# Kernel tuning notes

Hardware: AMD Instinct MI355X
Metric: run time of the kernel (lower is better)

Reference implementation:

```python
import jax, jax.numpy as jnp
from jax import lax
import numpy as np

DIM = 512      # latent channel dim
K = 1024       # codebook size
KS = 320       # conv kernel size (== stride -> non-overlapping frames)
STRIDE = 320
B, L = 16, 160000  # 10s of 16kHz audio


def setup_inputs() -> dict:
    key = jax.random.key(0)
    ks = jax.random.split(key, 8)
    wav = jax.random.normal(ks[0], (B, 1, L), jnp.float32)
    enc_w = jax.random.normal(ks[1], (DIM, 1, KS), jnp.float32) * 0.05
    enc_b = jnp.zeros((DIM,), jnp.float32)
    codebook = jax.random.normal(ks[2], (K, DIM), jnp.float32)
    lin_w = jax.random.normal(ks[3], (DIM, DIM), jnp.float32) * 0.02
    lin_b = jnp.zeros((DIM,), jnp.float32)
    film_w = jax.random.normal(ks[4], (2 * DIM, DIM), jnp.float32) * 0.02
    film_b = jnp.zeros((2 * DIM,), jnp.float32)
    dec_w = jax.random.normal(ks[5], (DIM, 1, KS), jnp.float32) * 0.05
    dec_b = jnp.zeros((1,), jnp.float32)
    return dict(wav=wav, enc_w=enc_w, enc_b=enc_b, codebook=codebook,
                lin_w=lin_w, lin_b=lin_b, film_w=film_w, film_b=film_b,
                dec_w=dec_w, dec_b=dec_b)


def reference(wav, enc_w, enc_b, codebook, lin_w, lin_b, film_w, film_b, dec_w, dec_b):
    # --- NAC encoder: strided Conv1d, wav [B,1,L] -> emb [B,D,T] ---
    emb = lax.conv_general_dilated(
        wav, enc_w, window_strides=(STRIDE,), padding='VALID',
        dimension_numbers=('NCH', 'OIH', 'NCH')) + enc_b[None, :, None]

    # --- time-averaged embedding for conditioning ---
    time_avg = emb.mean(axis=-1)  # [B, D]

    # --- VQ encode: nearest codebook entry per frame ---
    x = emb.transpose(0, 2, 1)  # [B, T, D]
    # squared L2 distances [B, T, K]
    dist = (x * x).sum(-1, keepdims=True) \
         - 2.0 * jnp.einsum('btd,kd->btk', x, codebook) \
         + (codebook * codebook).sum(-1)
    codes = jnp.argmin(dist, axis=-1)  # [B, T] int

    # --- VQ decode: codebook gather ---
    emb_r = codebook[codes].transpose(0, 2, 1)  # [B, D, T]

    # --- linear on pooled embedding ---
    cond = time_avg @ lin_w.T + lin_b  # [B, D]

    # --- FiLM modulation: gamma * x + beta per channel ---
    gb = cond @ film_w.T + film_b      # [B, 2D]
    gamma, beta = jnp.split(gb, 2, axis=-1)
    modulated = gamma[:, :, None] * emb_r + beta[:, :, None]  # [B, D, T]

    # --- NAC decoder: transposed Conv1d back to waveform [B,1,L] ---
    out = lax.conv_transpose(
        modulated, dec_w, strides=(STRIDE,), padding='VALID',
        dimension_numbers=('NCH', 'IOH', 'NCH')) + dec_b[None, :, None]
    return out
```

## Files before the change

kernel.cpp:

```cpp
#include <hip/hip_runtime.h>

#define FR   8000
#define FRP  8192
#define DD   512
#define CK   1024
#define KSZ  320
#define TT   500
#define NB   16

typedef unsigned int u32;
typedef unsigned short u16;
typedef __attribute__((ext_vector_type(8))) short b8;
typedef __attribute__((ext_vector_type(4))) float f4;

__device__ __forceinline__ float bf2f(u16 h) {
    u32 u = ((u32)h) << 16;
    return __builtin_bit_cast(float, u);
}
__device__ __forceinline__ u16 f2bf(float f) {
    u32 u = __builtin_bit_cast(u32, f);
    u32 r = u + 0x7FFFu + ((u >> 16) & 1u);
    return (u16)(r >> 16);
}

__device__ __forceinline__ void gld16(const u16* g, u16* s) {
    __builtin_amdgcn_global_load_lds(
        (const __attribute__((address_space(1))) u32*)g,
        (__attribute__((address_space(3))) u32*)s, 16, 0, 0);
}

__device__ __forceinline__ f4 mfma(b8 a, b8 b, f4 c) {
    return __builtin_amdgcn_mfma_f32_16x16x32_bf16(a, b, c, 0, 0, 0);
}

__device__ __forceinline__ void split8(float4 a, float4 b, u16* dh, u16* dl) {
    float xs[8] = {a.x, a.y, a.z, a.w, b.x, b.y, b.z, b.w};
    union { u16 u[8]; b8 v; } H, L;
#pragma unroll
    for (int i = 0; i < 8; ++i) {
        u16 h = f2bf(xs[i]);
        H.u[i] = h;
        L.u[i] = f2bf(xs[i] - bf2f(h));
    }
    *(b8*)dh = H.v;
    *(b8*)dl = L.v;
}

__global__ __launch_bounds__(256) void k_prep(const float* __restrict__ enc_w,
                                              u16* __restrict__ ewh, u16* __restrict__ ewl,
                                              const float* __restrict__ cb,
                                              u16* __restrict__ cbh, u16* __restrict__ cbl,
                                              const float* __restrict__ dw,
                                              u16* __restrict__ dwfh, u16* __restrict__ dwfl,
                                              float* __restrict__ cbn,
                                              const float* __restrict__ wav,
                                              u16* __restrict__ wavh, u16* __restrict__ wavl,
                                              float* __restrict__ tsum) {
    const int bid = blockIdx.x, tid = threadIdx.x;
    if (bid < 80) {
        int i = (bid * 256 + tid) * 8;
        float4 a = *(const float4*)&enc_w[i];
        float4 b = *(const float4*)&enc_w[i + 4];
        split8(a, b, &ewh[i], &ewl[i]);
    } else if (bid < 336) {
        int i = ((bid - 80) * 256 + tid) * 8;
        float4 a = *(const float4*)&cb[i];
        float4 b = *(const float4*)&cb[i + 4];
        split8(a, b, &cbh[i], &cbl[i]);
    } else if (bid < 368) {
        int c = (bid - 336) * 32 + (tid >> 3);
        int l = tid & 7;
        float s = 0.f;
        for (int j = l * 4; j < DD; j += 32) {
            float4 v = *(const float4*)&cb[c * DD + j];
            s += v.x * v.x + v.y * v.y + v.z * v.z + v.w * v.w;
        }
        s += __shfl_xor(s, 1);
        s += __shfl_xor(s, 2);
        s += __shfl_xor(s, 4);
        if (l == 0) cbn[c] = s;
    } else if (bid < 1618) {
        int i = ((bid - 368) * 256 + tid) * 8;
        float4 a = *(const float4*)&wav[i];
        float4 b = *(const float4*)&wav[i + 4];
        split8(a, b, &wavh[i], &wavl[i]);
    } else if (bid < 1666) {
        int bid2 = bid - 1618;
        int d0 = (bid2 & 7) * 64;
        int sb = bid2 >> 3;
        int s0 = sb * 64;
        if (sb == 5) {
            b8 z = {};
#pragma unroll
            for (int k = 0; k < 2; ++k) {
                int lin = tid * 2 + k;
                int row = 320 + (lin >> 3);
                int col = (lin & 7) * 8;
                *(b8*)&dwfh[(size_t)row * DD + d0 + col] = z;
                *(b8*)&dwfl[(size_t)row * DD + d0 + col] = z;
            }
            return;
        }
        __shared__ float t64[64][68];
        const int u0 = 256 - s0;
#pragma unroll
        for (int p = 0; p < 4; ++p) {
            int row = (tid >> 4) + 16 * p;
            int c4 = (tid & 15) * 4;
            float4 v = *(const float4*)&dw[(size_t)(d0 + row) * KSZ + u0 + c4];
            t64[row][c4] = v.x; t64[row][c4 + 1] = v.y;
            t64[row][c4 + 2] = v.z; t64[row][c4 + 3] = v.w;
        }
        __syncthreads();
        const int i = tid >> 2;
        const int jq = (tid & 3) * 16;
        union { u16 u[8]; b8 v; } H0, L0, H1, L1;
#pragma unroll
        for (int j = 0; j < 8; ++j) {
            float m = t64[jq + j][63 - i];
            u16 h = f2bf(m);
            H0.u[j] = h; L0.u[j] = f2bf(m - bf2f(h));
            float m2 = t64[jq + 8 + j][63 - i];
            u16 h2 = f2bf(m2);
            H1.u[j] = h2; L1.u[j] = f2bf(m2 - bf2f(h2));
        }
        size_t o = (size_t)(s0 + i) * DD + d0 + jq;
        *(b8*)&dwfh[o] = H0.v; *(b8*)&dwfh[o + 8] = H1.v;
        *(b8*)&dwfl[o] = L0.v; *(b8*)&dwfl[o + 8] = L1.v;
    } else {
        float4 z = {0.f, 0.f, 0.f, 0.f};
#pragma unroll
        for (int k = 0; k < 8; ++k)
            *(float4*)&tsum[(tid * 8 + k) * 4] = z;
    }
}

#define PIPELINE(NT, STRIDE)                                                  \
    stg(0, 0);                                                                \
    stg(1, STRIDE);                                                           \
    int cur = 0;                                                              \
    for (int t = 0; t < NT; ++t) {                                            \
        if (t < NT - 1) asm volatile("s_waitcnt vmcnt(8)" ::: "memory");      \
        else            asm volatile("s_waitcnt vmcnt(0)" ::: "memory");      \
        __builtin_amdgcn_s_barrier();                                         \
        asm volatile("" ::: "memory");                                        \
        compute(cur);                                                         \
        asm volatile("" ::: "memory");                                        \
        __builtin_amdgcn_s_barrier();                                         \
        if (t < NT - 2) stg(cur, (t + 2) * STRIDE);                           \
        cur ^= 1;                                                             \
    }

__global__ __launch_bounds__(256, 2) void k_enc(const u16* __restrict__ Ahg,
                                                const u16* __restrict__ Alg,
                                                const u16* __restrict__ Bhg,
                                                const u16* __restrict__ Blg,
                                                const float* __restrict__ eb,
                                                u16* __restrict__ embh,
                                                u16* __restrict__ embl,
                                                float* __restrict__ tsum) {
    __shared__ __align__(16) u16 Ah[2][4096], Al[2][4096], Bh[2][4096], Bl[2][4096];
    __shared__ float tred[2][128][2];
    const int tid = threadIdx.x;
    const int l = tid & 63, w = tid >> 6, wm = w >> 1, wn = w & 1;
    const int lane16 = l & 15, laneK = l >> 4;
    const int g = blockIdx.x;
    const int xcd = g & 7, slot = g >> 3;
    const int f0 = (xcd * 8 + (slot & 7)) * 128;
    const int d0 = (slot >> 3) * 128;

    const int p0 = w * 128 + l, p1 = p0 + 64;
    const int r0 = p0 >> 2, q0 = (p0 & 3) ^ ((r0 >> 1) & 3);
    const int r1 = p1 >> 2, q1 = (p1 & 3) ^ ((r1 >> 1) & 3);
    int fa0 = f0 + r0; if (fa0 > FR - 1) fa0 = FR - 1;
    int fa1 = f0 + r1; if (fa1 > FR - 1) fa1 = FR - 1;
    const u16* gA0h = Ahg + (size_t)fa0 * KSZ + q0 * 8;
    const u16* gA1h = Ahg + (size_t)fa1 * KSZ + q1 * 8;
    const u16* gA0l = Alg + (size_t)fa0 * KSZ + q0 * 8;
    const u16* gA1l = Alg + (size_t)fa1 * KSZ + q1 * 8;
    const u16* gB0h = Bhg + (size_t)(d0 + r0) * KSZ + q0 * 8;
    const u16* gB1h = Bhg + (size_t)(d0 + r1) * KSZ + q1 * 8;
    const u16* gB0l = Blg + (size_t)(d0 + r0) * KSZ + q0 * 8;
    const u16* gB1l = Blg + (size_t)(d0 + r1) * KSZ + q1 * 8;

    int offA[4], offB[4];
#pragma unroll
    for (int i = 0; i < 4; ++i) {
        int ra = wm * 64 + i * 16 + lane16;
        offA[i] = (ra * 4 + (laneK ^ ((ra >> 1) & 3))) * 8;
        int rb = wn * 64 + i * 16 + lane16;
        offB[i] = (rb * 4 + (laneK ^ ((rb >> 1) & 3))) * 8;
    }

    f4 zero = {0.f, 0.f, 0.f, 0.f};
    f4 acc[4][4];
#pragma unroll
    for (int i = 0; i < 4; ++i)
#pragma unroll
        for (int j = 0; j < 4; ++j) acc[i][j] = zero;

    auto stg = [&](int buf, int kt) {
        gld16(gA0h + kt, Ah[buf] + w * 1024);
        gld16(gA1h + kt, Ah[buf] + w * 1024 + 512);
        gld16(gA0l + kt, Al[buf] + w * 1024);
        gld16(gA1l + kt, Al[buf] + w * 1024 + 512);
        gld16(gB0h + kt, Bh[buf] + w * 1024);
        gld16(gB1h + kt, Bh[buf] + w * 1024 + 512);
        gld16(gB0l + kt, Bl[buf] + w * 1024);
        gld16(gB1l + kt, Bl[buf] + w * 1024 + 512);
    };
    auto compute = [&](int buf) {
        b8 ah[4], al[4], bh[4], bl[4];
#pragma unroll
        for (int i = 0; i < 4; ++i) {
            ah[i] = *(const b8*)(Ah[buf] + offA[i]);
            al[i] = *(const b8*)(Al[buf] + offA[i]);
            bh[i] = *(const b8*)(Bh[buf] + offB[i]);
            bl[i] = *(const b8*)(Bl[buf] + offB[i]);
        }
#pragma unroll
        for (int mi = 0; mi < 4; ++mi)
#pragma unroll
            for (int ni = 0; ni < 4; ++ni) {
                acc[mi][ni] = mfma(ah[mi], bh[ni], acc[mi][ni]);
                acc[mi][ni] = mfma(ah[mi], bl[ni], acc[mi][ni]);
                acc[mi][ni] = mfma(al[mi], bh[ni], acc[mi][ni]);
            }
    };

    PIPELINE(10, 32)

    float ebv[4];
#pragma unroll
    for (int ni = 0; ni < 4; ++ni) ebv[ni] = eb[d0 + wn * 64 + ni * 16 + lane16];

    const int bA = f0 / TT;
    const int fB = min((bA + 1) * TT, f0 + 128);
    float sumA[4] = {}, sumB[4] = {};
#pragma unroll
    for (int mi = 0; mi < 4; ++mi)
#pragma unroll
        for (int q = 0; q < 4; ++q) {
            int f = f0 + wm * 64 + mi * 16 + laneK * 4 + q;
            bool live = f < FR;
            bool sideA = f < fB;
#pragma unroll
            for (int ni = 0; ni < 4; ++ni) {
                int d = d0 + wn * 64 + ni * 16 + lane16;
                float v = acc[mi][ni][q] + ebv[ni];
                u16 h = f2bf(v);
                size_t o = (size_t)f * DD + d;
                embh[o] = h;
                embl[o] = f2bf(v - bf2f(h));
                if (live) { if (sideA) sumA[ni] += v; else sumB[ni] += v; }
            }
        }
#pragma unroll
    for (int m = 16; m <= 32; m <<= 1)
#pragma unroll
        for (int ni = 0; ni < 4; ++ni) {
            sumA[ni] += __shfl_xor(sumA[ni], m);
            sumB[ni] += __shfl_xor(sumB[ni], m);
        }
    if (laneK == 0)
#pragma unroll
        for (int ni = 0; ni < 4; ++ni) {
            tred[wm][wn * 64 + ni * 16 + lane16][0] = sumA[ni];
            tred[wm][wn * 64 + ni * 16 + lane16][1] = sumB[ni];
        }
    __syncthreads();
    if (tid < 128 && bA < NB) {
        float a = tred[0][tid][0] + tred[1][tid][0];
        int d = d0 + tid;
        atomicAdd(&tsum[bA * DD + d], a);
        if (fB < f0 + 128 && bA + 1 < NB) {
            float b = tred[0][tid][1] + tred[1][tid][1];
            atomicAdd(&tsum[(bA + 1) * DD + d], b);
        }
    }
}

__global__ __launch_bounds__(256) void k_cond(const float* __restrict__ tsum,
                                              const float* __restrict__ lw,
                                              const float* __restrict__ lb,
                                              float* __restrict__ cond) {
    __shared__ float stv[NB * DD];
    const float inv = 1.0f / TT;
    for (int i = threadIdx.x * 4; i < NB * DD; i += 1024) {
        float4 v = *(const float4*)&tsum[i];
        v.x *= inv; v.y *= inv; v.z *= inv; v.w *= inv;
        *(float4*)&stv[i] = v;
    }
    __syncthreads();
    const int w = threadIdx.x >> 6, lane = threadIdx.x & 63;
    const int row = blockIdx.x * 4 + w;
    float wv[8];
#pragma unroll
    for (int j = 0; j < 8; ++j) wv[j] = lw[(size_t)row * DD + lane + 64 * j];
    float r[NB];
#pragma unroll
    for (int b = 0; b < NB; ++b) {
        float s = 0.f;
#pragma unroll
        for (int j = 0; j < 8; ++j) s += wv[j] * stv[b * DD + lane + 64 * j];
        r[b] = s;
    }
#pragma unroll
    for (int m = 32; m >= 1; m >>= 1)
#pragma unroll
        for (int b = 0; b < NB; ++b) r[b] += __shfl_xor(r[b], m);
    if (lane < NB) cond[lane * DD + row] = r[lane] + lb[row];
}

__global__ __launch_bounds__(256) void k_film(const float* __restrict__ cond,
                                              const float* __restrict__ fw,
                                              const float* __restrict__ fb,
                                              float* __restrict__ gbv) {
    __shared__ float sc[NB * DD];
    for (int i = threadIdx.x * 4; i < NB * DD; i += 1024)
        *(float4*)&sc[i] = *(const float4*)&cond[i];
    __syncthreads();
    const int w = threadIdx.x >> 6, lane = threadIdx.x & 63;
    const int row = blockIdx.x * 4 + w;
    float wv[8];
#pragma unroll
    for (int j = 0; j < 8; ++j) wv[j] = fw[(size_t)row * DD + lane + 64 * j];
    float r[NB];
#pragma unroll
    for (int b = 0; b < NB; ++b) {
        float s = 0.f;
#pragma unroll
        for (int j = 0; j < 8; ++j) s += wv[j] * sc[b * DD + lane + 64 * j];
        r[b] = s;
    }
#pragma unroll
    for (int m = 32; m >= 1; m >>= 1)
#pragma unroll
        for (int b = 0; b < NB; ++b) r[b] += __shfl_xor(r[b], m);
    if (lane < NB) gbv[lane * 2 * DD + row] = r[lane] + fb[row];
}

__global__ __launch_bounds__(256, 2) void k_dist(const u16* __restrict__ Ahg,
                                                 const u16* __restrict__ Alg,
                                                 const u16* __restrict__ Bhg,
                                                 const u16* __restrict__ Blg,
                                                 const float* __restrict__ cbn,
                                                 float* __restrict__ pmin,
                                                 int* __restrict__ pidx) {
    __shared__ __align__(16) u16 Ah[2][4096], Al[2][4096], Bh[2][4096], Bl[2][4096];
    __shared__ float s_best[128][2];
    __shared__ int s_bidx[128][2];
    const int tid = threadIdx.x;
    const int l = tid & 63, w = tid >> 6, wm = w >> 1, wn = w & 1;
    const int lane16 = l & 15, laneK = l >> 4;
    const int g = blockIdx.x;
    const int xcd = g & 7, slot = g >> 3;
    const int f0 = (xcd * 8 + (slot & 7)) * 128;
    const int cy = slot >> 3;
    const int c0 = cy * 128;

    const int p0 = w * 128 + l, p1 = p0 + 64;
    const int r0 = p0 >> 2, q0 = (p0 & 3) ^ ((r0 >> 1) & 3);
    const int r1 = p1 >> 2, q1 = (p1 & 3) ^ ((r1 >> 1) & 3);
    const u16* gA0h = Ahg + (size_t)(f0 + r0) * DD + q0 * 8;
    const u16* gA1h = Ahg + (size_t)(f0 + r1) * DD + q1 * 8;
    const u16* gA0l = Alg + (size_t)(f0 + r0) * DD + q0 * 8;
    const u16* gA1l = Alg + (size_t)(f0 + r1) * DD + q1 * 8;
    const u16* gB0h = Bhg + (size_t)(c0 + r0) * DD + q0 * 8;
    const u16* gB1h = Bhg + (size_t)(c0 + r1) * DD + q1 * 8;
    const u16* gB0l = Blg + (size_t)(c0 + r0) * DD + q0 * 8;
    const u16* gB1l = Blg + (size_t)(c0 + r1) * DD + q1 * 8;

    int offA[4], offB[4];
#pragma unroll
    for (int i = 0; i < 4; ++i) {
        int ra = wm * 64 + i * 16 + lane16;
        offA[i] = (ra * 4 + (laneK ^ ((ra >> 1) & 3))) * 8;
        int rb = wn * 64 + i * 16 + lane16;
        offB[i] = (rb * 4 + (laneK ^ ((rb >> 1) & 3))) * 8;
    }

    f4 zero = {0.f, 0.f, 0.f, 0.f};
    f4 acc[4][4];
#pragma unroll
    for (int i = 0; i < 4; ++i)
#pragma unroll
        for (int j = 0; j < 4; ++j) acc[i][j] = zero;

    auto stg = [&](int buf, int kt) {
        gld16(gA0h + kt, Ah[buf] + w * 1024);
        gld16(gA1h + kt, Ah[buf] + w * 1024 + 512);
        gld16(gA0l + kt, Al[buf] + w * 1024);
        gld16(gA1l + kt, Al[buf] + w * 1024 + 512);
        gld16(gB0h + kt, Bh[buf] + w * 1024);
        gld16(gB1h + kt, Bh[buf] + w * 1024 + 512);
        gld16(gB0l + kt, Bl[buf] + w * 1024);
        gld16(gB1l + kt, Bl[buf] + w * 1024 + 512);
    };
    auto compute = [&](int buf) {
        b8 ah[4], al[4], bh[4], bl[4];
#pragma unroll
        for (int i = 0; i < 4; ++i) {
            ah[i] = *(const b8*)(Ah[buf] + offA[i]);
            al[i] = *(const b8*)(Al[buf] + offA[i]);
            bh[i] = *(const b8*)(Bh[buf] + offB[i]);
            bl[i] = *(const b8*)(Bl[buf] + offB[i]);
        }
#pragma unroll
        for (int mi = 0; mi < 4; ++mi)
#pragma unroll
            for (int ni = 0; ni < 4; ++ni) {
                acc[mi][ni] = mfma(ah[mi], bh[ni], acc[mi][ni]);
                acc[mi][ni] = mfma(ah[mi], bl[ni], acc[mi][ni]);
                acc[mi][ni] = mfma(al[mi], bh[ni], acc[mi][ni]);
            }
    };

    PIPELINE(16, 32)

    float cbv[4];
    int cidx[4];
#pragma unroll
    for (int ni = 0; ni < 4; ++ni) {
        cidx[ni] = c0 + wn * 64 + ni * 16 + lane16;
        cbv[ni] = cbn[cidx[ni]];
    }
#pragma unroll
    for (int mi = 0; mi < 4; ++mi)
#pragma unroll
        for (int q = 0; q < 4; ++q) {
            float best = 3.4e38f;
            int bi = 0x7fffffff;
#pragma unroll
            for (int ni = 0; ni < 4; ++ni) {
                float s = cbv[ni] - 2.0f * acc[mi][ni][q];
                if (s < best || (s == best && cidx[ni] < bi)) { best = s; bi = cidx[ni]; }
            }
#pragma unroll
            for (int m = 8; m >= 1; m >>= 1) {
                float os = __shfl_xor(best, m);
                int oi = __shfl_xor(bi, m);
                if (os < best || (os == best && oi < bi)) { best = os; bi = oi; }
            }
            if (lane16 == 0) {
                int rl = wm * 64 + mi * 16 + laneK * 4 + q;
                s_best[rl][wn] = best;
                s_bidx[rl][wn] = bi;
            }
        }
    __syncthreads();
    if (tid < 128) {
        float b0 = s_best[tid][0], b1 = s_best[tid][1];
        int i0 = s_bidx[tid][0], i1 = s_bidx[tid][1];
        bool t1 = (b1 < b0) || (b1 == b0 && i1 < i0);
        int f = f0 + tid;
        if (f < FR) {
            pmin[f * 8 + cy] = t1 ? b1 : b0;
            pidx[f * 8 + cy] = t1 ? i1 : i0;
        }
    }
}

struct AV {
    float4 c00, c01, g00, g01, e00, e01;
    float4 c10, c11, g10, g11, e10, e11;
};

__global__ __launch_bounds__(256, 2) void k_dec(const float* __restrict__ pmin,
                                                const int* __restrict__ pidx,
                                                const float* __restrict__ cb,
                                                const float* __restrict__ gbv,
                                                const u16* __restrict__ Bhg,
                                                const u16* __restrict__ Blg,
                                                const float* __restrict__ db,
                                                float* __restrict__ out) {
    __shared__ __align__(16) u16 Ah[2][4096], Al[2][4096], Bh[2][4096], Bl[2][4096];
    __shared__ int codes_lds[128];
    __shared__ int b_lds[128];
    const int tid = threadIdx.x;
    const int l = tid & 63, w = tid >> 6, wm = w >> 1, wn = w & 1;
    const int lane16 = l & 15, laneK = l >> 4;
    const int f0 = blockIdx.y * 128, s0 = blockIdx.x * 128;

    if (tid < 128) {
        int f = f0 + tid;
        int fc = (f < FR) ? f : FR - 1;
        float best = pmin[fc * 8];
        int bi = pidx[fc * 8];
#pragma unroll
        for (int y = 1; y < 8; ++y) {
            float s = pmin[fc * 8 + y];
            if (s < best) { best = s; bi = pidx[fc * 8 + y]; }
        }
        codes_lds[tid] = bi;
        b_lds[tid] = fc / TT;
    }
    __syncthreads();

    const int p0 = w * 128 + l, p1 = p0 + 64;
    const int r0 = p0 >> 2, q0 = (p0 & 3) ^ ((r0 >> 1) & 3);
    const int r1 = p1 >> 2, q1 = (p1 & 3) ^ ((r1 >> 1) & 3);
    const u16* gB0h = Bhg + (size_t)(s0 + r0) * DD + q0 * 8;
    const u16* gB1h = Bhg + (size_t)(s0 + r1) * DD + q1 * 8;
    const u16* gB0l = Blg + (size_t)(s0 + r0) * DD + q0 * 8;
    const u16* gB1l = Blg + (size_t)(s0 + r1) * DD + q1 * 8;

    const int pa0 = tid, pa1 = tid + 256;
    const int ra0 = pa0 >> 2, qa0 = (pa0 & 3) ^ ((ra0 >> 1) & 3);
    const int ra1 = pa1 >> 2, qa1 = (pa1 & 3) ^ ((ra1 >> 1) & 3);
    const float* cp0 = cb + (size_t)codes_lds[ra0] * DD + qa0 * 8;
    const float* cp1 = cb + (size_t)codes_lds[ra1] * DD + qa1 * 8;
    const float* gp0 = gbv + b_lds[ra0] * 2 * DD + qa0 * 8;
    const float* gp1 = gbv + b_lds[ra1] * 2 * DD + qa1 * 8;

    int offA[4], offB[4];
#pragma unroll
    for (int i = 0; i < 4; ++i) {
        int ra = wm * 64 + i * 16 + lane16;
        offA[i] = (ra * 4 + (laneK ^ ((ra >> 1) & 3))) * 8;
        int rb = wn * 64 + i * 16 + lane16;
        offB[i] = (rb * 4 + (laneK ^ ((rb >> 1) & 3))) * 8;
    }

    f4 zero = {0.f, 0.f, 0.f, 0.f};
    f4 acc[4][4];
#pragma unroll
    for (int i = 0; i < 4; ++i)
#pragma unroll
        for (int j = 0; j < 4; ++j) acc[i][j] = zero;

    auto stgB = [&](int buf, int kt) {
        gld16(gB0h + kt, Bh[buf] + w * 1024);
        gld16(gB1h + kt, Bh[buf] + w * 1024 + 512);
        gld16(gB0l + kt, Bl[buf] + w * 1024);
        gld16(gB1l + kt, Bl[buf] + w * 1024 + 512);
    };
    auto loadA = [&](int kt) {
        AV v;
        v.c00 = *(const float4*)(cp0 + kt);
        v.c01 = *(const float4*)(cp0 + kt + 4);
        v.g00 = *(const float4*)(gp0 + kt);
        v.g01 = *(const float4*)(gp0 + kt + 4);
        v.e00 = *(const float4*)(gp0 + DD + kt);
        v.e01 = *(const float4*)(gp0 + DD + kt + 4);
        v.c10 = *(const float4*)(cp1 + kt);
        v.c11 = *(const float4*)(cp1 + kt + 4);
        v.g10 = *(const float4*)(gp1 + kt);
        v.g11 = *(const float4*)(gp1 + kt + 4);
        v.e10 = *(const float4*)(gp1 + DD + kt);
        v.e11 = *(const float4*)(gp1 + DD + kt + 4);
        return v;
    };
    auto writeA = [&](int buf, const AV& v) {
        float4 m00, m01, m10, m11;
        m00.x = v.g00.x * v.c00.x + v.e00.x; m00.y = v.g00.y * v.c00.y + v.e00.y;
        m00.z = v.g00.z * v.c00.z + v.e00.z; m00.w = v.g00.w * v.c00.w + v.e00.w;
        m01.x = v.g01.x * v.c01.x + v.e01.x; m01.y = v.g01.y * v.c01.y + v.e01.y;
        m01.z = v.g01.z * v.c01.z + v.e01.z; m01.w = v.g01.w * v.c01.w + v.e01.w;
        m10.x = v.g10.x * v.c10.x + v.e10.x; m10.y = v.g10.y * v.c10.y + v.e10.y;
        m10.z = v.g10.z * v.c10.z + v.e10.z; m10.w = v.g10.w * v.c10.w + v.e10.w;
        m11.x = v.g11.x * v.c11.x + v.e11.x; m11.y = v.g11.y * v.c11.y + v.e11.y;
        m11.z = v.g11.z * v.c11.z + v.e11.z; m11.w = v.g11.w * v.c11.w + v.e11.w;
        split8(m00, m01, Ah[buf] + pa0 * 8, Al[buf] + pa0 * 8);
        split8(m10, m11, Ah[buf] + pa1 * 8, Al[buf] + pa1 * 8);
    };
    auto compute = [&](int buf) {
        b8 ah[4], al[4], bh[4], bl[4];
#pragma unroll
        for (int i = 0; i < 4; ++i) {
            ah[i] = *(const b8*)(Ah[buf] + offA[i]);
            al[i] = *(const b8*)(Al[buf] + offA[i]);
            bh[i] = *(const b8*)(Bh[buf] + offB[i]);
            bl[i] = *(const b8*)(Bl[buf] + offB[i]);
        }
#pragma unroll
        for (int mi = 0; mi < 4; ++mi)
#pragma unroll
            for (int ni = 0; ni < 4; ++ni) {
                acc[mi][ni] = mfma(ah[mi], bh[ni], acc[mi][ni]);
                acc[mi][ni] = mfma(ah[mi], bl[ni], acc[mi][ni]);
                acc[mi][ni] = mfma(al[mi], bh[ni], acc[mi][ni]);
            }
    };

    {
        AV v0 = loadA(0);
        AV v1 = loadA(32);
        stgB(0, 0);
        stgB(1, 32);
        writeA(0, v0);
        writeA(1, v1);
    }
    int cur = 0;
    for (int t = 0; t < 16; ++t) {
        if (t < 15) asm volatile("s_waitcnt vmcnt(4) lgkmcnt(0)" ::: "memory");
        else        asm volatile("s_waitcnt vmcnt(0) lgkmcnt(0)" ::: "memory");
        __builtin_amdgcn_s_barrier();
        asm volatile("" ::: "memory");
        compute(cur);
        asm volatile("" ::: "memory");
        __builtin_amdgcn_s_barrier();
        if (t < 14) {
            AV v = loadA((t + 2) * 32);
            stgB(cur, (t + 2) * 32);
            writeA(cur, v);
        }
        cur ^= 1;
    }

    const float d0v = db[0];
#pragma unroll
    for (int mi = 0; mi < 4; ++mi)
#pragma unroll
        for (int q = 0; q < 4; ++q) {
            int f = f0 + wm * 64 + mi * 16 + laneK * 4 + q;
            if (f < FR) {
#pragma unroll
                for (int ni = 0; ni < 4; ++ni) {
                    int s = s0 + wn * 64 + ni * 16 + lane16;
                    if (s < KSZ) out[(size_t)f * KSZ + s] = acc[mi][ni][q] + d0v;
                }
            }
        }
}

extern "C" void kernel_launch(void* const* d_in, const int* in_sizes, int n_in,
                              void* d_out, int out_size, void* d_ws, size_t ws_size,
                              hipStream_t stream) {
    const float* wav    = (const float*)d_in[0];
    const float* enc_w  = (const float*)d_in[1];
    const float* enc_b  = (const float*)d_in[2];
    const float* cb     = (const float*)d_in[3];
    const float* lin_w  = (const float*)d_in[4];
    const float* lin_b  = (const float*)d_in[5];
    const float* film_w = (const float*)d_in[6];
    const float* film_b = (const float*)d_in[7];
    const float* dec_w  = (const float*)d_in[8];
    const float* dec_b  = (const float*)d_in[9];
    float* out = (float*)d_out;

    char* p = (char*)d_ws;
    u16* embh = (u16*)p;                 p += (size_t)FRP * DD * 2;
    u16* embl = (u16*)p;                 p += (size_t)FRP * DD * 2;
    u16* wavh = (u16*)p;                 p += (size_t)FR * KSZ * 2;
    u16* wavl = (u16*)p;                 p += (size_t)FR * KSZ * 2;
    u16* ewh  = (u16*)p;                 p += (size_t)DD * KSZ * 2;
    u16* ewl  = (u16*)p;                 p += (size_t)DD * KSZ * 2;
    u16* cbh  = (u16*)p;                 p += (size_t)CK * DD * 2;
    u16* cbl  = (u16*)p;                 p += (size_t)CK * DD * 2;
    u16* dwfh = (u16*)p;                 p += (size_t)384 * DD * 2;
    u16* dwfl = (u16*)p;                 p += (size_t)384 * DD * 2;
    float* cbn  = (float*)p;             p += CK * 4;
    float* tsum = (float*)p;             p += NB * DD * 4;
    float* cond = (float*)p;             p += NB * DD * 4;
    float* gbv  = (float*)p;             p += NB * 2 * DD * 4;
    float* pmin = (float*)p;             p += FR * 8 * 4;
    int*   pidx = (int*)p;               p += FR * 8 * 4;

    k_prep<<<dim3(1667), 256, 0, stream>>>(enc_w, ewh, ewl, cb, cbh, cbl,
                                           dec_w, dwfh, dwfl, cbn, wav, wavh, wavl, tsum);
    k_enc<<<dim3(256), 256, 0, stream>>>(wavh, wavl, ewh, ewl, enc_b, embh, embl, tsum);
    k_cond<<<dim3(128), 256, 0, stream>>>(tsum, lin_w, lin_b, cond);
    k_film<<<dim3(256), 256, 0, stream>>>(cond, film_w, film_b, gbv);
    k_dist<<<dim3(512), 256, 0, stream>>>(embh, embl, cbh, cbl, cbn, pmin, pidx);
    k_dec<<<dim3(3, 63), 256, 0, stream>>>(pmin, pidx, cb, gbv, dwfh, dwfl, dec_b, out);
}
```

Baseline: 172.9 us.

## Load MFMA operands directly from global memory in distance kernel, dropping LDS staging

```diff
diff --git a/kernel.cpp b/kernel.cpp
--- a/kernel.cpp
+++ b/kernel.cpp
@@ -347,37 +347,28 @@
                                                  const float* __restrict__ cbn,
                                                  float* __restrict__ pmin,
                                                  int* __restrict__ pidx) {
-    __shared__ __align__(16) u16 Ah[2][4096], Al[2][4096], Bh[2][4096], Bl[2][4096];
     __shared__ float s_best[128][2];
     __shared__ int s_bidx[128][2];
     const int tid = threadIdx.x;
     const int l = tid & 63, w = tid >> 6, wm = w >> 1, wn = w & 1;
     const int lane16 = l & 15, laneK = l >> 4;
     const int g = blockIdx.x;
-    const int xcd = g & 7, slot = g >> 3;
-    const int f0 = (xcd * 8 + (slot & 7)) * 128;
-    const int cy = slot >> 3;
-    const int c0 = cy * 128;
-
-    const int p0 = w * 128 + l, p1 = p0 + 64;
-    const int r0 = p0 >> 2, q0 = (p0 & 3) ^ ((r0 >> 1) & 3);
-    const int r1 = p1 >> 2, q1 = (p1 & 3) ^ ((r1 >> 1) & 3);
-    const u16* gA0h = Ahg + (size_t)(f0 + r0) * DD + q0 * 8;
-    const u16* gA1h = Ahg + (size_t)(f0 + r1) * DD + q1 * 8;
-    const u16* gA0l = Alg + (size_t)(f0 + r0) * DD + q0 * 8;
-    const u16* gA1l = Alg + (size_t)(f0 + r1) * DD + q1 * 8;
-    const u16* gB0h = Bhg + (size_t)(c0 + r0) * DD + q0 * 8;
-    const u16* gB1h = Bhg + (size_t)(c0 + r1) * DD + q1 * 8;
-    const u16* gB0l = Blg + (size_t)(c0 + r0) * DD + q0 * 8;
-    const u16* gB1l = Blg + (size_t)(c0 + r1) * DD + q1 * 8;
-
-    int offA[4], offB[4];
+    const int xcd = g & 7, loc = g >> 3;
+    const int cy = loc >> 3;
+    const int fpl = loc & 7;
+    const int fbase = (xcd * 8 + fpl) * 128;
+    const int f0 = fbase + wm * 64;
+    const int c0 = cy * 128 + wn * 64;
+
+    const u16 *pah[4], *pal[4], *pbh[4], *pbl[4];
 #pragma unroll
     for (int i = 0; i < 4; ++i) {
-        int ra = wm * 64 + i * 16 + lane16;
-        offA[i] = (ra * 4 + (laneK ^ ((ra >> 1) & 3))) * 8;
-        int rb = wn * 64 + i * 16 + lane16;
-        offB[i] = (rb * 4 + (laneK ^ ((rb >> 1) & 3))) * 8;
+        int ra = f0 + i * 16 + lane16;
+        pah[i] = Ahg + (size_t)ra * DD + laneK * 8;
+        pal[i] = Alg + (size_t)ra * DD + laneK * 8;
+        int rb = c0 + i * 16 + lane16;
+        pbh[i] = Bhg + (size_t)rb * DD + laneK * 8;
+        pbl[i] = Blg + (size_t)rb * DD + laneK * 8;
     }
 
     f4 zero = {0.f, 0.f, 0.f, 0.f};
@@ -387,42 +378,31 @@
 #pragma unroll
         for (int j = 0; j < 4; ++j) acc[i][j] = zero;
 
-    auto stg = [&](int buf, int kt) {
-        gld16(gA0h + kt, Ah[buf] + w * 1024);
-        gld16(gA1h + kt, Ah[buf] + w * 1024 + 512);
-        gld16(gA0l + kt, Al[buf] + w * 1024);
-        gld16(gA1l + kt, Al[buf] + w * 1024 + 512);
-        gld16(gB0h + kt, Bh[buf] + w * 1024);
-        gld16(gB1h + kt, Bh[buf] + w * 1024 + 512);
-        gld16(gB0l + kt, Bl[buf] + w * 1024);
-        gld16(gB1l + kt, Bl[buf] + w * 1024 + 512);
-    };
-    auto compute = [&](int buf) {
-        b8 ah[4], al[4], bh[4], bl[4];
-#pragma unroll
-        for (int i = 0; i < 4; ++i) {
-            ah[i] = *(const b8*)(Ah[buf] + offA[i]);
-            al[i] = *(const b8*)(Al[buf] + offA[i]);
-            bh[i] = *(const b8*)(Bh[buf] + offB[i]);
-            bl[i] = *(const b8*)(Bl[buf] + offB[i]);
-        }
-#pragma unroll
-        for (int mi = 0; mi < 4; ++mi)
+    for (int kt = 0; kt < DD; kt += 32) {
+        b8 bh[4], bl[4];
+#pragma unroll
+        for (int ni = 0; ni < 4; ++ni) {
+            bh[ni] = *(const b8*)(pbh[ni] + kt);
+            bl[ni] = *(const b8*)(pbl[ni] + kt);
+        }
+#pragma unroll
+        for (int mi = 0; mi < 4; ++mi) {
+            b8 ah = *(const b8*)(pah[mi] + kt);
+            b8 al = *(const b8*)(pal[mi] + kt);
 #pragma unroll
             for (int ni = 0; ni < 4; ++ni) {
-                acc[mi][ni] = mfma(ah[mi], bh[ni], acc[mi][ni]);
-                acc[mi][ni] = mfma(ah[mi], bl[ni], acc[mi][ni]);
-                acc[mi][ni] = mfma(al[mi], bh[ni], acc[mi][ni]);
-            }
-    };
-
-    PIPELINE(16, 32)
+                acc[mi][ni] = mfma(ah, bh[ni], acc[mi][ni]);
+                acc[mi][ni] = mfma(ah, bl[ni], acc[mi][ni]);
+                acc[mi][ni] = mfma(al, bh[ni], acc[mi][ni]);
+            }
+        }
+    }
 
     float cbv[4];
     int cidx[4];
 #pragma unroll
     for (int ni = 0; ni < 4; ++ni) {
-        cidx[ni] = c0 + wn * 64 + ni * 16 + lane16;
+        cidx[ni] = c0 + ni * 16 + lane16;
         cbv[ni] = cbn[cidx[ni]];
     }
 #pragma unroll
@@ -453,7 +433,7 @@
         float b0 = s_best[tid][0], b1 = s_best[tid][1];
         int i0 = s_bidx[tid][0], i1 = s_bidx[tid][1];
         bool t1 = (b1 < b0) || (b1 == b0 && i1 < i0);
-        int f = f0 + tid;
+        int f = fbase + tid;
         if (f < FR) {
             pmin[f * 8 + cy] = t1 ? b1 : b0;
             pidx[f * 8 + cy] = t1 ? i1 : i0;
```

New measurement: 209.5 us. 21.1% more time.
